# Kernel optimization log

Measured on AMD Instinct MI355X. Metric: run time of the kernel, lower is better.

The kernel has to match this reference:

```python
import jax, jax.numpy as jnp
import numpy as np
import math

K = 20        # args.k  (global-branch neighbors)
KL = 20       # args.kl (local-branch neighbors)
EPS = 1e-5    # BatchNorm eps
SLOPE = 0.2   # LeakyReLU slope


def _knn(x, k, keep):
    # x: [B,C,N]; keep: [B,N] bool column mask. pd = -||xi - xj||^2.
    xx = jnp.sum(x * x, axis=1)                          # [B,N]
    inner = jnp.einsum('bci,bcj->bij', x, x)             # [B,N,N]
    pd = 2.0 * inner - xx[:, :, None] - xx[:, None, :]
    mn = jnp.min(pd, axis=-1)                            # per-row min
    # suppressed columns are set to the row min so topk never selects them
    pd = jnp.where(keep[:, None, :], pd, mn[:, :, None])
    return jax.lax.top_k(pd, k)[1]                       # [B,N,k]


def _gather(pts, idx):
    # pts: [B,N,C], idx: [B,N,k] -> [B,N,k,C]
    b = jnp.arange(pts.shape[0])[:, None, None]
    return pts[b, idx]


def _edge_feat(x, k, keep, smooth):
    # DGCNN edge features: concat(neighbor - center, center) -> [B,2C,N,k]
    idx = _knn(x, k, keep)
    xp = jnp.transpose(x, (0, 2, 1))                     # [B,N,C]
    if smooth:
        # GraphLayer: neighbors come from a topk-mean smoothed field
        knn_x = _gather(xp, idx)                         # [B,N,k,C]
        k2 = math.ceil(k * 2 / 3)
        top = jax.lax.top_k(jnp.transpose(knn_x, (0, 1, 3, 2)), k2)[0]
        src = jnp.mean(top, axis=-1)                     # [B,N,C]
    else:
        src = xp
    feat = _gather(src, idx)                             # [B,N,k,C]
    ctr = jnp.broadcast_to(xp[:, :, None, :], feat.shape)
    out = jnp.concatenate([feat - ctr, ctr], axis=-1)    # [B,N,k,2C]
    return jnp.transpose(out, (0, 3, 1, 2))


def _bn(y, axes):
    # BatchNorm (training-mode batch stats, gamma=1, beta=0 as at init)
    mu = jnp.mean(y, axis=axes, keepdims=True)
    var = jnp.var(y, axis=axes, keepdims=True)
    return (y - mu) * jax.lax.rsqrt(var + EPS)


def _conv_block(x, w, axes):
    # 1x1 conv (no bias) + BN + LeakyReLU
    ein = 'oc,bcnk->bonk' if x.ndim == 4 else 'oc,bcn->bon'
    return jax.nn.leaky_relu(_bn(jnp.einsum(ein, w, x), axes), SLOPE)


def _forward(x, local_idx, w1, w2, w3, w4, w5, w6, w7, w8, w9,
             l1w, l2w, l2b, l3w, l3b):
    keep_l = local_idx
    keep_g = jnp.logical_not(local_idx)
    ax4 = (0, 2, 3)
    # local (smoothed GraphLayer) branch, neighbors restricted to local points
    xl1 = _conv_block(_edge_feat(x,   KL, keep_l, True), w1, ax4).max(-1)
    xl2 = _conv_block(_edge_feat(xl1, KL, keep_l, True), w2, ax4).max(-1)
    xl3 = _conv_block(_edge_feat(xl2, KL, keep_l, True), w3, ax4).max(-1)
    xl4 = _conv_block(_edge_feat(xl3, KL, keep_l, True), w4, ax4).max(-1)
    x_local = jnp.concatenate([xl1, xl2, xl3, xl4], axis=1)  # [B,512,N]
    # global branch, neighbors restricted to non-local points
    xg1 = _conv_block(_edge_feat(x,   K, keep_g, False), w5, ax4).max(-1)
    xg2 = _conv_block(_edge_feat(xg1, K, keep_g, False), w6, ax4).max(-1)
    xg3 = _conv_block(_edge_feat(xg2, K, keep_g, False), w7, ax4).max(-1)
    xg4 = _conv_block(_edge_feat(xg3, K, keep_g, False), w8, ax4).max(-1)
    x_glob = jnp.concatenate([xg1, xg2, xg3, xg4], axis=1)   # [B,512,N]
    # per-point merge: local columns take the local-branch features
    h = jnp.where(local_idx[:, None, :], x_local, x_glob)
    h = _conv_block(h, w9, (0, 2))                            # [B,E,N]
    g = jnp.concatenate([h.max(-1), h.mean(-1)], axis=1)      # [B,2E]
    # head: linears + BN1d + LeakyReLU; dropout is identity (eval mode)
    g = jax.nn.leaky_relu(_bn(g @ l1w.T, (0,)), SLOPE)
    g = jax.nn.leaky_relu(_bn(g @ l2w.T + l2b, (0,)), SLOPE)
    return g @ l3w.T + l3b


def setup_inputs() -> dict:
    key = jax.random.key(0)
    ks = jax.random.split(key, 16)
    B, N, E, OUT = 4, 2048, 1024, 40

    def w(k, o, i):
        return jax.random.normal(k, (o, i), jnp.float32) / np.sqrt(i)

    return {
        'x': jax.random.normal(ks[0], (B, 3, N), jnp.float32),
        'local_idx': jax.random.bernoulli(ks[1], 0.5, (B, N)),
        'geod_dist': jax.random.normal(ks[2], (B, N), jnp.float32),
        'w1': w(ks[3], 64, 6),   'w2': w(ks[4], 64, 128),
        'w3': w(ks[5], 128, 128), 'w4': w(ks[6], 256, 256),
        'w5': w(ks[7], 64, 6),   'w6': w(ks[8], 64, 128),
        'w7': w(ks[9], 128, 128), 'w8': w(ks[10], 256, 256),
        'w9': w(ks[11], E, 512),
        'l1w': w(ks[12], 512, 2 * E),
        'l2w': w(ks[13], 256, 512),
        'l2b': jnp.zeros((256,), jnp.float32),
        'l3w': w(ks[14], OUT, 256),
        'l3b': jnp.zeros((OUT,), jnp.float32),
    }


def reference(x, local_idx, geod_dist, w1, w2, w3, w4, w5, w6, w7, w8, w9,
              l1w, l2w, l2b, l3w, l3b):
    del geod_dist  # accepted but unused in the original forward
    return _forward(x, local_idx, w1, w2, w3, w4, w5, w6, w7, w8, w9,
                    l1w, l2w, l2b, l3w, l3b)
```

## Files before the change

kernel.cpp:

```cpp
#include <hip/hip_runtime.h>
#include <hip/hip_bf16.h>
#include <cfloat>

#define BB 4
#define NN 2048
#define KNN 20
#define KTOP 14
#define EPSBN 1e-5f
#define SLOPE 0.2f

__global__ void k_xx3(const float* __restrict__ x, float* __restrict__ xx) {
  int t = blockIdx.x * 64 + threadIdx.x;
  int b = t >> 11, n = t & 2047;
  const float* xb = x + (long)b * (3L * NN) + n;
  float v0 = xb[0], v1 = xb[NN], v2 = xb[2 * NN];
  xx[t] = v0 * v0 + v1 * v1 + v2 * v2;
}

__device__ __forceinline__ void sel_pass(const float* __restrict__ trow,
                                         const int* __restrict__ lrow,
                                         int keepv, float mn, int lane,
                                         int* __restrict__ orow) {
  int base = 4 * lane;
  float v[8][4];
#pragma unroll
  for (int q = 0; q < 8; ++q) {
    float4 lv = *(const float4*)(trow + 256 * q + base);
    int4 kv = *(const int4*)(lrow + 256 * q + base);
    v[q][0] = (((kv.x != 0) ? 1 : 0) == keepv) ? lv.x : mn;
    v[q][1] = (((kv.y != 0) ? 1 : 0) == keepv) ? lv.y : mn;
    v[q][2] = (((kv.z != 0) ? 1 : 0) == keepv) ? lv.z : mn;
    v[q][3] = (((kv.w != 0) ? 1 : 0) == keepv) ? lv.w : mn;
  }
  for (int t = 0; t < KNN; ++t) {
    float bv = -FLT_MAX; int bj = NN;
#pragma unroll
    for (int q = 0; q < 8; ++q)
#pragma unroll
      for (int e = 0; e < 4; ++e) {
        int j = 256 * q + base + e;
        if (v[q][e] > bv) { bv = v[q][e]; bj = j; }
      }
#pragma unroll
    for (int d = 1; d < 64; d <<= 1) {
      float ov = __shfl_xor(bv, d);
      int oj = __shfl_xor(bj, d);
      if (ov > bv || (ov == bv && oj < bj)) { bv = ov; bj = oj; }
    }
    if (lane == 0) orow[t] = bj;
#pragma unroll
    for (int q = 0; q < 8; ++q)
#pragma unroll
      for (int e = 0; e < 4; ++e) {
        int j = 256 * q + base + e;
        if (j == bj) v[q][e] = -FLT_MAX;
      }
  }
}

template <int C>
__global__ __launch_bounds__(256) void k_knn(
    const float* __restrict__ xbase, long bstride, const float* __restrict__ xxbase,
    const int* __restrict__ lidx, int keepv,
    int* __restrict__ idxA, int* __restrict__ idxB ) {
  __shared__ float tile[4][NN];
  __shared__ float a_lds[C][4];
  int b = blockIdx.y;
  int i0 = blockIdx.x * 4;
  const float* xb = xbase + (long)b * bstride;
  const float* xxb = xxbase + b * NN;
  int tid = threadIdx.x;
  for (int t = tid; t < 4 * C; t += 256) {
    int c = t >> 2, r = t & 3;
    a_lds[c][r] = xb[(long)c * NN + i0 + r];
  }
  __syncthreads();
  for (int jt = 0; jt < NN; jt += 1024) {
    float acc[4][4];
#pragma unroll
    for (int r = 0; r < 4; ++r)
#pragma unroll
      for (int s = 0; s < 4; ++s) acc[r][s] = 0.f;
#pragma unroll 4
    for (int c = 0; c < C; ++c) {
      float4 a = *(const float4*)&a_lds[c][0];
      float4 h = *(const float4*)&xb[(long)c * NN + jt + tid * 4];
      acc[0][0] += a.x * h.x; acc[0][1] += a.x * h.y; acc[0][2] += a.x * h.z; acc[0][3] += a.x * h.w;
      acc[1][0] += a.y * h.x; acc[1][1] += a.y * h.y; acc[1][2] += a.y * h.z; acc[1][3] += a.y * h.w;
      acc[2][0] += a.z * h.x; acc[2][1] += a.z * h.y; acc[2][2] += a.z * h.z; acc[2][3] += a.z * h.w;
      acc[3][0] += a.w * h.x; acc[3][1] += a.w * h.y; acc[3][2] += a.w * h.z; acc[3][3] += a.w * h.w;
    }
    float4 xxj = *(const float4*)&xxb[jt + tid * 4];
#pragma unroll
    for (int r = 0; r < 4; ++r) {
      float xxi = xxb[i0 + r];
      float4 o;
      o.x = 2.f * acc[r][0] - xxi - xxj.x;
      o.y = 2.f * acc[r][1] - xxi - xxj.y;
      o.z = 2.f * acc[r][2] - xxi - xxj.z;
      o.w = 2.f * acc[r][3] - xxi - xxj.w;
      *(float4*)&tile[r][jt + tid * 4] = o;
    }
  }
  __syncthreads();
  int wid = tid >> 6, lane = tid & 63;
  const float* trow = &tile[wid][0];
  const int* lrow = lidx + b * NN;
  float mn = FLT_MAX;
#pragma unroll
  for (int q = 0; q < 8; ++q) {
    float4 lv = *(const float4*)(trow + 256 * q + 4 * lane);
    mn = fminf(mn, fminf(fminf(lv.x, lv.y), fminf(lv.z, lv.w)));
  }
#pragma unroll
  for (int d = 1; d < 64; d <<= 1) mn = fminf(mn, __shfl_xor(mn, d));
  int i = i0 + wid;
  sel_pass(trow, lrow, keepv, mn, lane, idxA + ((long)b * NN + i) * KNN);
  if (idxB)
    sel_pass(trow, lrow, 1 - keepv, mn, lane, idxB + ((long)b * NN + i) * KNN);
}

__global__ void k_smooth(const float* __restrict__ x, long bstride, int C,
                         const int* __restrict__ idx, float* __restrict__ src) {
  long t = (long)blockIdx.x * blockDim.x + threadIdx.x;
  if (t >= (long)BB * C * NN) return;
  int n = (int)(t % NN);
  int c = (int)((t / NN) % C);
  int b = (int)(t / ((long)NN * C));
  const int* id = idx + ((long)b * NN + n) * KNN;
  const float* xb = x + (long)b * bstride + (long)c * NN;
  float v[KNN]; float sum = 0.f;
#pragma unroll
  for (int kk = 0; kk < KNN; ++kk) { v[kk] = xb[id[kk]]; sum += v[kk]; }
  int r0 = -1, r1 = -1, r2 = -1, r3 = -1, r4 = -1, r5 = -1;
#pragma unroll
  for (int r = 0; r < KNN - KTOP; ++r) {
    float mvv = FLT_MAX; int mi = -1;
#pragma unroll
    for (int j = 0; j < KNN; ++j) {
      if (j == r0 || j == r1 || j == r2 || j == r3 || j == r4 || j == r5) continue;
      if (v[j] < mvv) { mvv = v[j]; mi = j; }
    }
    sum -= mvv;
    if (r == 0) r0 = mi; else if (r == 1) r1 = mi; else if (r == 2) r2 = mi;
    else if (r == 3) r3 = mi; else if (r == 4) r4 = mi; else r5 = mi;
  }
  src[((long)b * C + c) * NN + n] = sum * (1.f / KTOP);
}

__global__ void k_wprep_all(
    const float* __restrict__ w1, const float* __restrict__ w2,
    const float* __restrict__ w3, const float* __restrict__ w4,
    const float* __restrict__ w5, const float* __restrict__ w6,
    const float* __restrict__ w7, const float* __restrict__ w8,
    float* __restrict__ wa, float* __restrict__ wd) {
  int L = blockIdx.y;
  const float* w; int O, C; long off;
  switch (L) {
    case 0: w = w1; O = 64;  C = 3;   off = 0;     break;
    case 1: w = w2; O = 64;  C = 64;  off = 192;   break;
    case 2: w = w3; O = 128; C = 64;  off = 4288;  break;
    case 3: w = w4; O = 256; C = 128; off = 12480; break;
    case 4: w = w5; O = 64;  C = 3;   off = 45248; break;
    case 5: w = w6; O = 64;  C = 64;  off = 45440; break;
    case 6: w = w7; O = 128; C = 64;  off = 49536; break;
    default: w = w8; O = 256; C = 128; off = 57728; break;
  }
  for (int t = blockIdx.x * blockDim.x + threadIdx.x; t < O * C;
       t += gridDim.x * blockDim.x) {
    int o = t / C, c = t % C;
    float a = w[(long)o * 2 * C + c];
    float bb = w[(long)o * 2 * C + C + c];
    wa[off + (long)c * O + o] = a;
    wd[off + (long)c * O + o] = bb - a;
  }
}

template <int C>
__global__ __launch_bounds__(256) void k_zt2(
    const float* __restrict__ Ma, long mas,
    const float* __restrict__ Mb_, long mbs,
    const float* __restrict__ wa, const float* __restrict__ wd,
    int O, float* __restrict__ Zs, float* __restrict__ Zd) {
  constexpr int KC = (C >= 16) ? 16 : C;
  __shared__ float As[KC][64], Bs[KC][64];
  int z = blockIdx.z;
  int nyo = gridDim.y >> 1;
  int half = (blockIdx.y >= nyo) ? 1 : 0;
  int o0 = (half ? (blockIdx.y - nyo) : blockIdx.y) * 64;
  const float* M = half ? Mb_ : Ma;
  long ms = half ? mbs : mas;
  const float* Wt = half ? wd : wa;
  float* T = half ? Zd : Zs;
  const float* Mb = M + (long)z * ms;
  float* Tb = T + (long)z * NN * O;
  int tid = threadIdx.x;
  int tx = tid & 15, ty = tid >> 4;
  int n0 = blockIdx.x * 64;
  float acc[4][4];
#pragma unroll
  for (int r = 0; r < 4; ++r)
#pragma unroll
    for (int s = 0; s < 4; ++s) acc[r][s] = 0.f;
  for (int c0 = 0; c0 < C; c0 += KC) {
    for (int e = tid; e < KC * 64; e += 256) {
      int c = e >> 6, ii = e & 63;
      As[c][ii] = Mb[(long)(c0 + c) * NN + n0 + ii];
      Bs[c][ii] = Wt[(long)(c0 + c) * O + o0 + ii];
    }
    __syncthreads();
#pragma unroll
    for (int cc = 0; cc < KC; ++cc) {
      float4 a = *(const float4*)&As[cc][ty * 4];
      float4 h = *(const float4*)&Bs[cc][tx * 4];
      acc[0][0] += a.x * h.x; acc[0][1] += a.x * h.y; acc[0][2] += a.x * h.z; acc[0][3] += a.x * h.w;
      acc[1][0] += a.y * h.x; acc[1][1] += a.y * h.y; acc[1][2] += a.y * h.z; acc[1][3] += a.y * h.w;
      acc[2][0] += a.z * h.x; acc[2][1] += a.z * h.y; acc[2][2] += a.z * h.z; acc[2][3] += a.z * h.w;
      acc[3][0] += a.w * h.x; acc[3][1] += a.w * h.y; acc[3][2] += a.w * h.z; acc[3][3] += a.w * h.w;
    }
    __syncthreads();
  }
#pragma unroll
  for (int r = 0; r < 4; ++r) {
    float4 v; v.x = acc[r][0]; v.y = acc[r][1]; v.z = acc[r][2]; v.w = acc[r][3];
    *(float4*)&Tb[(long)(n0 + ty * 4 + r) * O + o0 + tx * 4] = v;
  }
}

template <int O, int PTS>
__global__ __launch_bounds__(O) void k_gmax(
    const float* __restrict__ Zs, const float* __restrict__ Zd,
    const int* __restrict__ idx, float* __restrict__ ymax,
    float* __restrict__ stats) {
  int tid = threadIdx.x;
  int bn0 = blockIdx.x * PTS;
  int b = bn0 >> 11;
  long zbase = (long)b * NN * O;
  float ss = 0.f, sq = 0.f;
  for (int p = 0; p < PTS; ++p) {
    int bn = bn0 + p;
    const int* ir = idx + (long)bn * KNN;
    float zd = Zd[(long)bn * O + tid];
    float smax = -FLT_MAX;
#pragma unroll
    for (int k = 0; k < KNN; ++k) {
      float y = Zs[zbase + (long)ir[k] * O + tid] + zd;
      smax = fmaxf(smax, y); ss += y; sq += y * y;
    }
    ymax[(long)bn * O + tid] = smax;
  }
  atomicAdd(&stats[tid], ss);
  atomicAdd(&stats[O + tid], sq);
}

__global__ void k_bnmax(const float* __restrict__ ymax, const float* __restrict__ stats,
                        int O, float invcnt, float* __restrict__ out, long out_bstride,
                        float* __restrict__ xxout) {
  long t = (long)blockIdx.x * blockDim.x + threadIdx.x;
  if (t >= (long)BB * O * NN) return;
  int n = (int)(t % NN);
  int o = (int)((t / NN) % O);
  int b = (int)(t / ((long)NN * O));
  float mu = stats[o] * invcnt;
  float var = stats[O + o] * invcnt - mu * mu;
  float rs = rsqrtf(var + EPSBN);
  float v = (ymax[((long)b * NN + n) * O + o] - mu) * rs;
  v = v >= 0.f ? v : SLOPE * v;
  out[(long)b * out_bstride + (long)o * NN + n] = v;
  if (xxout) atomicAdd(&xxout[b * NN + n], v * v);
}

__global__ __launch_bounds__(256) void k_gemm9(
    const float* __restrict__ W, const float* __restrict__ xl,
    const float* __restrict__ xg, const int* __restrict__ lidx,
    float* __restrict__ h2, float* __restrict__ stats) {
  __shared__ float Ws[16][68];
  __shared__ float Hs[16][68];
  int tid = threadIdx.x;
  int tx = tid & 15, ty = tid >> 4;
  int p0 = blockIdx.x * 64, o0 = blockIdx.y * 64;
  int b = p0 >> 11, n0 = p0 & 2047;
  int hp = tid & 63, cq = (tid >> 6) * 4;
  const float* hbase;
  {
    int pt = p0 + hp;
    hbase = (lidx[pt] ? xl : xg) + (long)b * (512L * NN) + (pt & 2047);
  }
  int wo = tid >> 2, wc = (tid & 3) * 4;
  float acc[4][4];
#pragma unroll
  for (int i = 0; i < 4; ++i)
#pragma unroll
    for (int j = 0; j < 4; ++j) acc[i][j] = 0.f;

  for (int c0 = 0; c0 < 512; c0 += 16) {
    float4 wv = *(const float4*)(W + (long)(o0 + wo) * 512 + c0 + wc);
    Ws[wc + 0][wo] = wv.x; Ws[wc + 1][wo] = wv.y;
    Ws[wc + 2][wo] = wv.z; Ws[wc + 3][wo] = wv.w;
    long crow = (long)(c0 + cq) * NN;
    Hs[cq + 0][hp] = hbase[crow];
    Hs[cq + 1][hp] = hbase[crow + NN];
    Hs[cq + 2][hp] = hbase[crow + 2 * NN];
    Hs[cq + 3][hp] = hbase[crow + 3 * NN];
    __syncthreads();
#pragma unroll
    for (int cc = 0; cc < 16; ++cc) {
      float4 a = *(const float4*)&Ws[cc][ty * 4];
      float4 h = *(const float4*)&Hs[cc][tx * 4];
      acc[0][0] += a.x * h.x; acc[0][1] += a.x * h.y; acc[0][2] += a.x * h.z; acc[0][3] += a.x * h.w;
      acc[1][0] += a.y * h.x; acc[1][1] += a.y * h.y; acc[1][2] += a.y * h.z; acc[1][3] += a.y * h.w;
      acc[2][0] += a.z * h.x; acc[2][1] += a.z * h.y; acc[2][2] += a.z * h.z; acc[2][3] += a.z * h.w;
      acc[3][0] += a.w * h.x; acc[3][1] += a.w * h.y; acc[3][2] += a.w * h.z; acc[3][3] += a.w * h.w;
    }
    __syncthreads();
  }
#pragma unroll
  for (int i = 0; i < 4; ++i) {
    int o = o0 + ty * 4 + i;
    float4 v; v.x = acc[i][0]; v.y = acc[i][1]; v.z = acc[i][2]; v.w = acc[i][3];
    *(float4*)&h2[((long)b * 1024 + o) * NN + n0 + tx * 4] = v;
    float ss = acc[i][0] + acc[i][1] + acc[i][2] + acc[i][3];
    float sq = acc[i][0] * acc[i][0] + acc[i][1] * acc[i][1] +
               acc[i][2] * acc[i][2] + acc[i][3] * acc[i][3];
    for (int d = 8; d > 0; d >>= 1) {
      ss += __shfl_down(ss, d, 16);
      sq += __shfl_down(sq, d, 16);
    }
    if (tx == 0) {
      atomicAdd(&stats[o], ss);
      atomicAdd(&stats[1024 + o], sq);
    }
  }
}

__global__ void k_gpool(const float* __restrict__ h2, const float* __restrict__ stats,
                        float* __restrict__ g) {
  int b = blockIdx.x / 1024, o = blockIdx.x % 1024;
  int tid = threadIdx.x;
  float mu = stats[o] * (1.f / 8192.f);
  float var = stats[1024 + o] * (1.f / 8192.f) - mu * mu;
  float rs = rsqrtf(var + EPSBN);
  const float* hr = h2 + ((long)b * 1024 + o) * NN;
  float mx = -FLT_MAX, sm = 0.f;
  for (int n = tid; n < NN; n += 256) {
    float v = (hr[n] - mu) * rs; v = v >= 0.f ? v : SLOPE * v;
    mx = fmaxf(mx, v); sm += v;
  }
  __shared__ float smx[256], ssm[256];
  smx[tid] = mx; ssm[tid] = sm; __syncthreads();
  for (int s = 128; s > 0; s >>= 1) {
    if (tid < s) { smx[tid] = fmaxf(smx[tid], smx[tid + s]); ssm[tid] += ssm[tid + s]; }
    __syncthreads();
  }
  if (tid == 0) { g[b * 2048 + o] = smx[0]; g[b * 2048 + 1024 + o] = ssm[0] * (1.f / NN); }
}

__global__ void k_head(const float* __restrict__ gin, int CIN, const float* __restrict__ wl,
                       const float* __restrict__ bias, float* __restrict__ gout, int do_bn) {
  int f = blockIdx.x, tid = threadIdx.x, F = gridDim.x;
  const float* wr = wl + (long)f * CIN;
  float a0 = 0, a1 = 0, a2 = 0, a3 = 0;
  for (int c = tid; c < CIN; c += 256) {
    float wv = wr[c];
    a0 += wv * gin[c];         a1 += wv * gin[CIN + c];
    a2 += wv * gin[2 * CIN + c]; a3 += wv * gin[3 * CIN + c];
  }
  __shared__ float s0[256], s1[256], s2[256], s3[256];
  s0[tid] = a0; s1[tid] = a1; s2[tid] = a2; s3[tid] = a3; __syncthreads();
  for (int s = 128; s > 0; s >>= 1) {
    if (tid < s) { s0[tid] += s0[tid + s]; s1[tid] += s1[tid + s];
                   s2[tid] += s2[tid + s]; s3[tid] += s3[tid + s]; }
    __syncthreads();
  }
  if (tid == 0) {
    float z0 = s0[0], z1 = s1[0], z2 = s2[0], z3 = s3[0];
    if (bias) { float bb = bias[f]; z0 += bb; z1 += bb; z2 += bb; z3 += bb; }
    if (do_bn) {
      float mu = 0.25f * (z0 + z1 + z2 + z3);
      float var = 0.25f * (z0 * z0 + z1 * z1 + z2 * z2 + z3 * z3) - mu * mu;
      float rs = rsqrtf(var + EPSBN);
      z0 = (z0 - mu) * rs; z1 = (z1 - mu) * rs; z2 = (z2 - mu) * rs; z3 = (z3 - mu) * rs;
      z0 = z0 >= 0.f ? z0 : SLOPE * z0; z1 = z1 >= 0.f ? z1 : SLOPE * z1;
      z2 = z2 >= 0.f ? z2 : SLOPE * z2; z3 = z3 >= 0.f ? z3 : SLOPE * z3;
    }
    gout[0 * F + f] = z0; gout[1 * F + f] = z1; gout[2 * F + f] = z2; gout[3 * F + f] = z3;
  }
}

extern "C" void kernel_launch(void* const* d_in, const int* in_sizes, int n_in,
                              void* d_out, int out_size, void* d_ws, size_t ws_size,
                              hipStream_t stream) {
  const float* x   = (const float*)d_in[0];
  const int*   lidx= (const int*)d_in[1];
  const float* w1  = (const float*)d_in[3];
  const float* w2  = (const float*)d_in[4];
  const float* w3  = (const float*)d_in[5];
  const float* w4  = (const float*)d_in[6];
  const float* w5  = (const float*)d_in[7];
  const float* w6  = (const float*)d_in[8];
  const float* w7  = (const float*)d_in[9];
  const float* w8  = (const float*)d_in[10];
  const float* w9  = (const float*)d_in[11];
  const float* l1w = (const float*)d_in[12];
  const float* l2w = (const float*)d_in[13];
  const float* l2b = (const float*)d_in[14];
  const float* l3w = (const float*)d_in[15];
  const float* l3b = (const float*)d_in[16];
  float* out = (float*)d_out;

  float* ws    = (float*)d_ws;
  float* xxall = ws;
  float* stats = ws + 57344;
  int*   idxb  = (int*)(ws + 61440);
  float* xloc  = ws + 225280;
  float* xglb  = ws + 4419584;
  float* big   = ws + 8613888;
  float* g     = ws + 17002496;
  float* g1    = ws + 17010688;
  float* g2    = ws + 17012736;
  float* waall = ws + 17013760;
  float* wdall = ws + 17104256;

  float* srcb  = big;
  float* Zs    = big + 1048576;
  float* Zd    = big + 3145728;
  float* ymaxb = big + 5242880;
  float* h2    = big;
  int*   idxG  = (int*)xglb;

  float* xxS0 = xxall;
  float* xxS1 = xxall + 8192;
  float* xxS2 = xxall + 16384;
  float* xxS3 = xxall + 24576;
  float* xxS4 = xxall + 32768;
  float* xxS5 = xxall + 40960;
  float* xxS6 = xxall + 49152;

  float* SL1 = stats + 0;    float* SL2 = stats + 128;
  float* SL3 = stats + 256;  float* SL4 = stats + 512;
  float* SG1 = stats + 1024; float* SG2 = stats + 1152;
  float* SG3 = stats + 1280; float* SG4 = stats + 1536;
  float* S9  = stats + 2048;

  const float invE = 1.f / (BB * NN * KNN);
  const long XS0 = 3L * NN;
  const long XS  = 512L * NN;
  const dim3 gknn(NN / 4, BB);

  hipMemsetAsync(ws, 0, 61440 * sizeof(float), stream);
  k_wprep_all<<<dim3(128, 8), 256, 0, stream>>>(w1, w2, w3, w4, w5, w6, w7, w8,
                                                waall, wdall);
  k_xx3<<<128, 64, 0, stream>>>(x, xxS0);

  k_knn<3><<<gknn, 256, 0, stream>>>(x, XS0, xxS0, lidx, 1, idxb, idxG);

  k_smooth<<<(BB * 3 * NN + 255) / 256, 256, 0, stream>>>(x, XS0, 3, idxb, srcb);
  k_zt2<3><<<dim3(32, 2, 4), 256, 0, stream>>>(srcb, 3L * NN, x, XS0,
                                               waall + 0, wdall + 0, 64, Zs, Zd);
  k_gmax<64, 8><<<BB * NN / 8, 64, 0, stream>>>(Zs, Zd, idxb, ymaxb, SL1);
  k_bnmax<<<(BB * 64 * NN + 255) / 256, 256, 0, stream>>>(ymaxb, SL1, 64, invE,
                                                          xloc + 0 * NN, XS, xxS1);
  k_knn<64><<<gknn, 256, 0, stream>>>(xloc, XS, xxS1, lidx, 1, idxb, nullptr);
  k_smooth<<<(BB * 64 * NN + 255) / 256, 256, 0, stream>>>(xloc, XS, 64, idxb, srcb);
  k_zt2<64><<<dim3(32, 2, 4), 256, 0, stream>>>(srcb, 64L * NN, xloc, XS,
                                                waall + 192, wdall + 192, 64, Zs, Zd);
  k_gmax<64, 8><<<BB * NN / 8, 64, 0, stream>>>(Zs, Zd, idxb, ymaxb, SL2);
  k_bnmax<<<(BB * 64 * NN + 255) / 256, 256, 0, stream>>>(ymaxb, SL2, 64, invE,
                                                          xloc + 64 * NN, XS, xxS2);
  k_knn<64><<<gknn, 256, 0, stream>>>(xloc + 64 * NN, XS, xxS2, lidx, 1, idxb, nullptr);
  k_smooth<<<(BB * 64 * NN + 255) / 256, 256, 0, stream>>>(xloc + 64 * NN, XS, 64, idxb, srcb);
  k_zt2<64><<<dim3(32, 4, 4), 256, 0, stream>>>(srcb, 64L * NN, xloc + 64 * NN, XS,
                                                waall + 4288, wdall + 4288, 128, Zs, Zd);
  k_gmax<128, 16><<<BB * NN / 16, 128, 0, stream>>>(Zs, Zd, idxb, ymaxb, SL3);
  k_bnmax<<<(BB * 128 * NN + 255) / 256, 256, 0, stream>>>(ymaxb, SL3, 128, invE,
                                                           xloc + 128 * NN, XS, xxS3);
  k_knn<128><<<gknn, 256, 0, stream>>>(xloc + 128 * NN, XS, xxS3, lidx, 1, idxb, nullptr);
  k_smooth<<<(BB * 128 * NN + 255) / 256, 256, 0, stream>>>(xloc + 128 * NN, XS, 128, idxb, srcb);
  k_zt2<128><<<dim3(32, 8, 4), 256, 0, stream>>>(srcb, 128L * NN, xloc + 128 * NN, XS,
                                                 waall + 12480, wdall + 12480, 256, Zs, Zd);
  k_gmax<256, 16><<<BB * NN / 16, 256, 0, stream>>>(Zs, Zd, idxb, ymaxb, SL4);
  k_bnmax<<<(BB * 256 * NN + 255) / 256, 256, 0, stream>>>(ymaxb, SL4, 256, invE,
                                                           xloc + 256 * NN, XS, nullptr);

  k_zt2<3><<<dim3(32, 2, 4), 256, 0, stream>>>(x, XS0, x, XS0,
                                               waall + 45248, wdall + 45248, 64, Zs, Zd);
  k_gmax<64, 8><<<BB * NN / 8, 64, 0, stream>>>(Zs, Zd, idxG, ymaxb, SG1);
  k_bnmax<<<(BB * 64 * NN + 255) / 256, 256, 0, stream>>>(ymaxb, SG1, 64, invE,
                                                          xglb + 0 * NN, XS, xxS4);
  k_knn<64><<<gknn, 256, 0, stream>>>(xglb, XS, xxS4, lidx, 0, idxb, nullptr);
  k_zt2<64><<<dim3(32, 2, 4), 256, 0, stream>>>(xglb, XS, xglb, XS,
                                                waall + 45440, wdall + 45440, 64, Zs, Zd);
  k_gmax<64, 8><<<BB * NN / 8, 64, 0, stream>>>(Zs, Zd, idxb, ymaxb, SG2);
  k_bnmax<<<(BB * 64 * NN + 255) / 256, 256, 0, stream>>>(ymaxb, SG2, 64, invE,
                                                          xglb + 64 * NN, XS, xxS5);
  k_knn<64><<<gknn, 256, 0, stream>>>(xglb + 64 * NN, XS, xxS5, lidx, 0, idxb, nullptr);
  k_zt2<64><<<dim3(32, 4, 4), 256, 0, stream>>>(xglb + 64 * NN, XS, xglb + 64 * NN, XS,
                                                waall + 49536, wdall + 49536, 128, Zs, Zd);
  k_gmax<128, 16><<<BB * NN / 16, 128, 0, stream>>>(Zs, Zd, idxb, ymaxb, SG3);
  k_bnmax<<<(BB * 128 * NN + 255) / 256, 256, 0, stream>>>(ymaxb, SG3, 128, invE,
                                                           xglb + 128 * NN, XS, xxS6);
  k_knn<128><<<gknn, 256, 0, stream>>>(xglb + 128 * NN, XS, xxS6, lidx, 0, idxb, nullptr);
  k_zt2<128><<<dim3(32, 8, 4), 256, 0, stream>>>(xglb + 128 * NN, XS, xglb + 128 * NN, XS,
                                                 waall + 57728, wdall + 57728, 256, Zs, Zd);
  k_gmax<256, 16><<<BB * NN / 16, 256, 0, stream>>>(Zs, Zd, idxb, ymaxb, SG4);
  k_bnmax<<<(BB * 256 * NN + 255) / 256, 256, 0, stream>>>(ymaxb, SG4, 256, invE,
                                                           xglb + 256 * NN, XS, nullptr);

  {
    dim3 g9(NN * BB / 64, 1024 / 64);
    k_gemm9<<<g9, 256, 0, stream>>>(w9, xloc, xglb, lidx, h2, S9);
  }
  k_gpool<<<BB * 1024, 256, 0, stream>>>(h2, S9, g);
  k_head<<<512, 256, 0, stream>>>(g, 2048, l1w, nullptr, g1, 1);
  k_head<<<256, 256, 0, stream>>>(g1, 512, l2w, l2b, g2, 1);
  k_head<<<40, 256, 0, stream>>>(g2, 256, l3w, l3b, out, 0);
}
```

Measured before the change: 1.486 ms.

## Keep kNN distance rows in registers per wave instead of shared-memory tile

The kNN kernel now has each wave compute its own query row of distances directly into registers (8x4 per lane) and select the top-20 from those registers. This removes the 32 KB shared tile, its store/load round trip and one barrier, which should raise occupancy. The cost is the loss of 4-row register blocking: every wave streams all C channels of the key points from global memory on its own, so global/L2 traffic per block rises about fourfold and register pressure goes up. A DUAL template parameter keeps the two-pass selection for the first layer only.

New measurement: 1.894 ms. +27.5%, slower.

```diff
diff --git a/kernel.cpp b/kernel.cpp
--- a/kernel.cpp
+++ b/kernel.cpp
@@ -17,28 +17,15 @@
   xx[t] = v0 * v0 + v1 * v1 + v2 * v2;
 }
 
-__device__ __forceinline__ void sel_pass(const float* __restrict__ trow,
-                                         const int* __restrict__ lrow,
-                                         int keepv, float mn, int lane,
-                                         int* __restrict__ orow) {
-  int base = 4 * lane;
-  float v[8][4];
-#pragma unroll
-  for (int q = 0; q < 8; ++q) {
-    float4 lv = *(const float4*)(trow + 256 * q + base);
-    int4 kv = *(const int4*)(lrow + 256 * q + base);
-    v[q][0] = (((kv.x != 0) ? 1 : 0) == keepv) ? lv.x : mn;
-    v[q][1] = (((kv.y != 0) ? 1 : 0) == keepv) ? lv.y : mn;
-    v[q][2] = (((kv.z != 0) ? 1 : 0) == keepv) ? lv.z : mn;
-    v[q][3] = (((kv.w != 0) ? 1 : 0) == keepv) ? lv.w : mn;
-  }
+__device__ __forceinline__ void sel20(float v[8][4], int lane,
+                                      int* __restrict__ orow) {
   for (int t = 0; t < KNN; ++t) {
     float bv = -FLT_MAX; int bj = NN;
 #pragma unroll
     for (int q = 0; q < 8; ++q)
 #pragma unroll
       for (int e = 0; e < 4; ++e) {
-        int j = 256 * q + base + e;
+        int j = 256 * q + 4 * lane + e;
         if (v[q][e] > bv) { bv = v[q][e]; bj = j; }
       }
 #pragma unroll
@@ -52,72 +39,92 @@
     for (int q = 0; q < 8; ++q)
 #pragma unroll
       for (int e = 0; e < 4; ++e) {
-        int j = 256 * q + base + e;
+        int j = 256 * q + 4 * lane + e;
         if (j == bj) v[q][e] = -FLT_MAX;
       }
   }
 }
 
-template <int C>
+template <int C, int DUAL>
 __global__ __launch_bounds__(256) void k_knn(
     const float* __restrict__ xbase, long bstride, const float* __restrict__ xxbase,
     const int* __restrict__ lidx, int keepv,
     int* __restrict__ idxA, int* __restrict__ idxB ) {
-  __shared__ float tile[4][NN];
-  __shared__ float a_lds[C][4];
+  __shared__ float a_lds[4][C];
   int b = blockIdx.y;
   int i0 = blockIdx.x * 4;
   const float* xb = xbase + (long)b * bstride;
   const float* xxb = xxbase + b * NN;
-  int tid = threadIdx.x;
+  int tid = threadIdx.x, wid = tid >> 6, lane = tid & 63;
   for (int t = tid; t < 4 * C; t += 256) {
-    int c = t >> 2, r = t & 3;
-    a_lds[c][r] = xb[(long)c * NN + i0 + r];
+    int r = t & 3, c = t >> 2;
+    a_lds[r][c] = xb[(long)c * NN + i0 + r];
   }
   __syncthreads();
-  for (int jt = 0; jt < NN; jt += 1024) {
-    float acc[4][4];
-#pragma unroll
-    for (int r = 0; r < 4; ++r)
-#pragma unroll
-      for (int s = 0; s < 4; ++s) acc[r][s] = 0.f;
-#pragma unroll 4
-    for (int c = 0; c < C; ++c) {
-      float4 a = *(const float4*)&a_lds[c][0];
-      float4 h = *(const float4*)&xb[(long)c * NN + jt + tid * 4];
-      acc[0][0] += a.x * h.x; acc[0][1] += a.x * h.y; acc[0][2] += a.x * h.z; acc[0][3] += a.x * h.w;
-      acc[1][0] += a.y * h.x; acc[1][1] += a.y * h.y; acc[1][2] += a.y * h.z; acc[1][3] += a.y * h.w;
-      acc[2][0] += a.z * h.x; acc[2][1] += a.z * h.y; acc[2][2] += a.z * h.z; acc[2][3] += a.z * h.w;
-      acc[3][0] += a.w * h.x; acc[3][1] += a.w * h.y; acc[3][2] += a.w * h.z; acc[3][3] += a.w * h.w;
-    }
-    float4 xxj = *(const float4*)&xxb[jt + tid * 4];
-#pragma unroll
-    for (int r = 0; r < 4; ++r) {
-      float xxi = xxb[i0 + r];
-      float4 o;
-      o.x = 2.f * acc[r][0] - xxi - xxj.x;
-      o.y = 2.f * acc[r][1] - xxi - xxj.y;
-      o.z = 2.f * acc[r][2] - xxi - xxj.z;
-      o.w = 2.f * acc[r][3] - xxi - xxj.w;
-      *(float4*)&tile[r][jt + tid * 4] = o;
-    }
-  }
-  __syncthreads();
-  int wid = tid >> 6, lane = tid & 63;
-  const float* trow = &tile[wid][0];
+  int i = i0 + wid;
+  int base = 4 * lane;
+  float acc[8][4];
+#pragma unroll
+  for (int q = 0; q < 8; ++q)
+#pragma unroll
+    for (int e = 0; e < 4; ++e) acc[q][e] = 0.f;
+  for (int c = 0; c < C; ++c) {
+    float a = a_lds[wid][c];
+#pragma unroll
+    for (int q = 0; q < 8; ++q) {
+      float4 h = *(const float4*)&xb[(long)c * NN + 256 * q + base];
+      acc[q][0] += a * h.x; acc[q][1] += a * h.y;
+      acc[q][2] += a * h.z; acc[q][3] += a * h.w;
+    }
+  }
+  float xxi = xxb[i];
+#pragma unroll
+  for (int q = 0; q < 8; ++q) {
+    float4 xxj = *(const float4*)&xxb[256 * q + base];
+    acc[q][0] = 2.f * acc[q][0] - xxi - xxj.x;
+    acc[q][1] = 2.f * acc[q][1] - xxi - xxj.y;
+    acc[q][2] = 2.f * acc[q][2] - xxi - xxj.z;
+    acc[q][3] = 2.f * acc[q][3] - xxi - xxj.w;
+  }
+  float mn = acc[0][0];
+#pragma unroll
+  for (int q = 0; q < 8; ++q)
+#pragma unroll
+    for (int e = 0; e < 4; ++e) mn = fminf(mn, acc[q][e]);
+#pragma unroll
+  for (int d = 1; d < 64; d <<= 1) mn = fminf(mn, __shfl_xor(mn, d));
   const int* lrow = lidx + b * NN;
-  float mn = FLT_MAX;
-#pragma unroll
-  for (int q = 0; q < 8; ++q) {
-    float4 lv = *(const float4*)(trow + 256 * q + 4 * lane);
-    mn = fminf(mn, fminf(fminf(lv.x, lv.y), fminf(lv.z, lv.w)));
-  }
-#pragma unroll
-  for (int d = 1; d < 64; d <<= 1) mn = fminf(mn, __shfl_xor(mn, d));
-  int i = i0 + wid;
-  sel_pass(trow, lrow, keepv, mn, lane, idxA + ((long)b * NN + i) * KNN);
-  if (idxB)
-    sel_pass(trow, lrow, 1 - keepv, mn, lane, idxB + ((long)b * NN + i) * KNN);
+  if (DUAL) {
+    float v[8][4];
+#pragma unroll
+    for (int q = 0; q < 8; ++q) {
+      int4 kv = *(const int4*)(lrow + 256 * q + base);
+      v[q][0] = (((kv.x != 0) ? 1 : 0) == keepv) ? acc[q][0] : mn;
+      v[q][1] = (((kv.y != 0) ? 1 : 0) == keepv) ? acc[q][1] : mn;
+      v[q][2] = (((kv.z != 0) ? 1 : 0) == keepv) ? acc[q][2] : mn;
+      v[q][3] = (((kv.w != 0) ? 1 : 0) == keepv) ? acc[q][3] : mn;
+    }
+    sel20(v, lane, idxA + ((long)b * NN + i) * KNN);
+#pragma unroll
+    for (int q = 0; q < 8; ++q) {
+      int4 kv = *(const int4*)(lrow + 256 * q + base);
+      v[q][0] = (((kv.x != 0) ? 1 : 0) == (1 - keepv)) ? acc[q][0] : mn;
+      v[q][1] = (((kv.y != 0) ? 1 : 0) == (1 - keepv)) ? acc[q][1] : mn;
+      v[q][2] = (((kv.z != 0) ? 1 : 0) == (1 - keepv)) ? acc[q][2] : mn;
+      v[q][3] = (((kv.w != 0) ? 1 : 0) == (1 - keepv)) ? acc[q][3] : mn;
+    }
+    sel20(v, lane, idxB + ((long)b * NN + i) * KNN);
+  } else {
+#pragma unroll
+    for (int q = 0; q < 8; ++q) {
+      int4 kv = *(const int4*)(lrow + 256 * q + base);
+      acc[q][0] = (((kv.x != 0) ? 1 : 0) == keepv) ? acc[q][0] : mn;
+      acc[q][1] = (((kv.y != 0) ? 1 : 0) == keepv) ? acc[q][1] : mn;
+      acc[q][2] = (((kv.z != 0) ? 1 : 0) == keepv) ? acc[q][2] : mn;
+      acc[q][3] = (((kv.w != 0) ? 1 : 0) == keepv) ? acc[q][3] : mn;
+    }
+    sel20(acc, lane, idxA + ((long)b * NN + i) * KNN);
+  }
 }
 
 __global__ void k_smooth(const float* __restrict__ x, long bstride, int C,
@@ -452,7 +459,7 @@
                                                 waall, wdall);
   k_xx3<<<128, 64, 0, stream>>>(x, xxS0);
 
-  k_knn<3><<<gknn, 256, 0, stream>>>(x, XS0, xxS0, lidx, 1, idxb, idxG);
+  k_knn<3, 1><<<gknn, 256, 0, stream>>>(x, XS0, xxS0, lidx, 1, idxb, idxG);
 
   k_smooth<<<(BB * 3 * NN + 255) / 256, 256, 0, stream>>>(x, XS0, 3, idxb, srcb);
   k_zt2<3><<<dim3(32, 2, 4), 256, 0, stream>>>(srcb, 3L * NN, x, XS0,
@@ -460,21 +467,21 @@
   k_gmax<64, 8><<<BB * NN / 8, 64, 0, stream>>>(Zs, Zd, idxb, ymaxb, SL1);
   k_bnmax<<<(BB * 64 * NN + 255) / 256, 256, 0, stream>>>(ymaxb, SL1, 64, invE,
                                                           xloc + 0 * NN, XS, xxS1);
-  k_knn<64><<<gknn, 256, 0, stream>>>(xloc, XS, xxS1, lidx, 1, idxb, nullptr);
+  k_knn<64, 0><<<gknn, 256, 0, stream>>>(xloc, XS, xxS1, lidx, 1, idxb, nullptr);
   k_smooth<<<(BB * 64 * NN + 255) / 256, 256, 0, stream>>>(xloc, XS, 64, idxb, srcb);
   k_zt2<64><<<dim3(32, 2, 4), 256, 0, stream>>>(srcb, 64L * NN, xloc, XS,
                                                 waall + 192, wdall + 192, 64, Zs, Zd);
   k_gmax<64, 8><<<BB * NN / 8, 64, 0, stream>>>(Zs, Zd, idxb, ymaxb, SL2);
   k_bnmax<<<(BB * 64 * NN + 255) / 256, 256, 0, stream>>>(ymaxb, SL2, 64, invE,
                                                           xloc + 64 * NN, XS, xxS2);
-  k_knn<64><<<gknn, 256, 0, stream>>>(xloc + 64 * NN, XS, xxS2, lidx, 1, idxb, nullptr);
+  k_knn<64, 0><<<gknn, 256, 0, stream>>>(xloc + 64 * NN, XS, xxS2, lidx, 1, idxb, nullptr);
   k_smooth<<<(BB * 64 * NN + 255) / 256, 256, 0, stream>>>(xloc + 64 * NN, XS, 64, idxb, srcb);
   k_zt2<64><<<dim3(32, 4, 4), 256, 0, stream>>>(srcb, 64L * NN, xloc + 64 * NN, XS,
                                                 waall + 4288, wdall + 4288, 128, Zs, Zd);
   k_gmax<128, 16><<<BB * NN / 16, 128, 0, stream>>>(Zs, Zd, idxb, ymaxb, SL3);
   k_bnmax<<<(BB * 128 * NN + 255) / 256, 256, 0, stream>>>(ymaxb, SL3, 128, invE,
                                                            xloc + 128 * NN, XS, xxS3);
-  k_knn<128><<<gknn, 256, 0, stream>>>(xloc + 128 * NN, XS, xxS3, lidx, 1, idxb, nullptr);
+  k_knn<128, 0><<<gknn, 256, 0, stream>>>(xloc + 128 * NN, XS, xxS3, lidx, 1, idxb, nullptr);
   k_smooth<<<(BB * 128 * NN + 255) / 256, 256, 0, stream>>>(xloc + 128 * NN, XS, 128, idxb, srcb);
   k_zt2<128><<<dim3(32, 8, 4), 256, 0, stream>>>(srcb, 128L * NN, xloc + 128 * NN, XS,
                                                  waall + 12480, wdall + 12480, 256, Zs, Zd);
@@ -487,19 +494,19 @@
   k_gmax<64, 8><<<BB * NN / 8, 64, 0, stream>>>(Zs, Zd, idxG, ymaxb, SG1);
   k_bnmax<<<(BB * 64 * NN + 255) / 256, 256, 0, stream>>>(ymaxb, SG1, 64, invE,
                                                           xglb + 0 * NN, XS, xxS4);
-  k_knn<64><<<gknn, 256, 0, stream>>>(xglb, XS, xxS4, lidx, 0, idxb, nullptr);
+  k_knn<64, 0><<<gknn, 256, 0, stream>>>(xglb, XS, xxS4, lidx, 0, idxb, nullptr);
   k_zt2<64><<<dim3(32, 2, 4), 256, 0, stream>>>(xglb, XS, xglb, XS,
                                                 waall + 45440, wdall + 45440, 64, Zs, Zd);
   k_gmax<64, 8><<<BB * NN / 8, 64, 0, stream>>>(Zs, Zd, idxb, ymaxb, SG2);
   k_bnmax<<<(BB * 64 * NN + 255) / 256, 256, 0, stream>>>(ymaxb, SG2, 64, invE,
                                                           xglb + 64 * NN, XS, xxS5);
-  k_knn<64><<<gknn, 256, 0, stream>>>(xglb + 64 * NN, XS, xxS5, lidx, 0, idxb, nullptr);
+  k_knn<64, 0><<<gknn, 256, 0, stream>>>(xglb + 64 * NN, XS, xxS5, lidx, 0, idxb, nullptr);
   k_zt2<64><<<dim3(32, 4, 4), 256, 0, stream>>>(xglb + 64 * NN, XS, xglb + 64 * NN, XS,
                                                 waall + 49536, wdall + 49536, 128, Zs, Zd);
   k_gmax<128, 16><<<BB * NN / 16, 128, 0, stream>>>(Zs, Zd, idxb, ymaxb, SG3);
   k_bnmax<<<(BB * 128 * NN + 255) / 256, 256, 0, stream>>>(ymaxb, SG3, 128, invE,
                                                            xglb + 128 * NN, XS, xxS6);
-  k_knn<128><<<gknn, 256, 0, stream>>>(xglb + 128 * NN, XS, xxS6, lidx, 0, idxb, nullptr);
+  k_knn<128, 0><<<gknn, 256, 0, stream>>>(xglb + 128 * NN, XS, xxS6, lidx, 0, idxb, nullptr);
   k_zt2<128><<<dim3(32, 8, 4), 256, 0, stream>>>(xglb + 128 * NN, XS, xglb + 128 * NN, XS,
                                                  waall + 57728, wdall + 57728, 256, Zs, Zd);
   k_gmax<256, 16><<<BB * NN / 16, 256, 0, stream>>>(Zs, Zd, idxb, ymaxb, SG4);
```
